# Performance work log

Hardware: AMD Instinct MI355X
Metric: run time of the kernel (lower is better)

## Reference

```python
import jax, jax.numpy as jnp
import numpy as np

B, F, L, E = 65536, 64, 32, 512  # batch, n_feat, n_latent, n_embed
LN_EPS = 1e-5


def setup_inputs() -> dict:
    key = jax.random.key(0)
    ks = jax.random.split(key, 9)
    s1 = 1.0 / np.sqrt(L)
    return {
        "batch_factors": jax.random.uniform(ks[0], (B, F), dtype=jnp.float32),
        "w_raw": jax.random.normal(ks[1], (F,), dtype=jnp.float32),
        "W1": jax.random.normal(ks[2], (F, L, L), dtype=jnp.float32) * s1,
        "b1": jax.random.normal(ks[3], (F, L), dtype=jnp.float32) * 0.01,
        "gamma": jnp.ones((F, L), dtype=jnp.float32),
        "beta": jnp.zeros((F, L), dtype=jnp.float32),
        "W2": jax.random.normal(ks[4], (F, L, E), dtype=jnp.float32) * s1,
        "b2": jax.random.normal(ks[5], (F, E), dtype=jnp.float32) * 0.01,
    }


def reference(batch_factors, w_raw, W1, b1, gamma, beta, W2, b2):
    half = L // 2
    freqs = 0.1 * (2.0 ** jnp.arange(half, dtype=batch_factors.dtype))  # [L/2]
    x = batch_factors[..., None]                                        # [B,F,1]
    enc = jnp.concatenate([jnp.sin(freqs * x), jnp.cos(freqs * x)], axis=-1)  # [B,F,L]

    # per-feature Linear -> LayerNorm -> GELU (dropout is identity in eval)
    h = jnp.einsum('bfi,fij->bfj', enc, W1) + b1                        # [B,F,L]
    mu = jnp.mean(h, axis=-1, keepdims=True)
    var = jnp.var(h, axis=-1, keepdims=True)
    h = (h - mu) * jax.lax.rsqrt(var + LN_EPS) * gamma + beta
    h = jax.nn.gelu(h, approximate=False)

    # softmax-weighted sum of per-feature Linear(L->E) outputs, fused so the
    # [B,F,E] intermediate is never materialized:
    w = jax.nn.softmax(w_raw)                                           # [F]
    batch_embed = jnp.einsum('bfj,fje->be', h * w[None, :, None], W2) + w @ b2  # [B,E]
    return (batch_embed, w)
```

## Files before the change

### kernel.cpp

```cpp
#include <hip/hip_runtime.h>
#include <hip/hip_bf16.h>
#include <cstdint>

#define B_N 65536
#define F_N 64
#define L_N 32
#define E_N 512

typedef short bf16x8 __attribute__((ext_vector_type(8)));
typedef float f32x4 __attribute__((ext_vector_type(4)));

__device__ __forceinline__ float gelu_fast(float v) {
  float z = fabsf(v) * 0.7071067811865476f;
  float p = fmaf(z, fmaf(z, fmaf(z, fmaf(z, 0.078108f, 0.000972f),
                                 0.230389f), 0.278393f), 1.0f);
  float p2 = p * p;
  float p4 = p2 * p2;
  float er = 1.0f - __builtin_amdgcn_rcpf(p4);
  float half_er = copysignf(0.5f * er, v);
  return v * (0.5f + half_er);
}

__device__ __forceinline__ float gelu_exact(float v) {
  float z  = v * 0.7071067811865476f;
  float az = fabsf(z);
  float t  = __builtin_amdgcn_rcpf(fmaf(0.3275911f, az, 1.0f));
  float p  = t * fmaf(t, fmaf(t, fmaf(t, fmaf(t, 1.061405429f, -1.453152027f),
                                      1.421413741f), -0.284496736f), 0.254829592f);
  float e    = __expf(-z * z);
  float erfa = fmaf(-p, e, 1.0f);
  float er   = (z < 0.0f) ? -erfa : erfa;
  return v * fmaf(0.5f, er, 0.5f);
}

__global__ __launch_bounds__(256) void k_pre(const float* __restrict__ w_raw,
                                             const float* __restrict__ b2,
                                             const float* __restrict__ W1,
                                             const float* __restrict__ W2,
                                             float* __restrict__ wb2,
                                             float* __restrict__ out_tail,
                                             uint4* __restrict__ W1T,
                                             uint4* __restrict__ W2T) {
  __shared__ float ls[64 * 65];
  int bb = blockIdx.x, tid = threadIdx.x;
  float m = -1e30f;
  for (int i = 0; i < F_N; i++) m = fmaxf(m, w_raw[i]);
  float s = 0.f;
  for (int i = 0; i < F_N; i++) s += expf(w_raw[i] - m);
  float inv_s = 1.0f / s;

  if (bb < 2) {
    int e = bb * 256 + tid;
    float a = 0.f;
    for (int f = 0; f < F_N; f++)
      a = fmaf(expf(w_raw[f] - m) * inv_s, b2[f * E_N + e], a);
    wb2[e] = a;
    if (bb == 0 && tid < F_N) out_tail[tid] = expf(w_raw[tid] - m) * inv_s;
  } else if (bb < 18) {
    int f = (bb - 2) * 4 + (tid >> 6);
    int lane = tid & 63, quad = lane >> 4, r16 = lane & 15;
#pragma unroll
    for (int jt = 0; jt < 2; jt++) {
      union { __hip_bfloat162 p[4]; uint4 u; } pk;
#pragma unroll
      for (int d = 0; d < 4; d++) {
        float lo = W1[f * 1024 + (quad * 4 + d) * 32 + jt * 16 + r16];
        float hi = W1[f * 1024 + (16 + quad * 4 + d) * 32 + jt * 16 + r16];
        pk.p[d] = __float22bfloat162_rn(make_float2(lo, hi));
      }
      W1T[(f * 2 + jt) * 64 + lane] = pk.u;
    }
  } else {
    int blk = bb - 18;
    int kt = blk >> 3, et = blk & 7;
    int k0 = kt * 64, e0 = et * 64;
#pragma unroll
    for (int i = 0; i < 16; i++) {
      int idx = i * 256 + tid;
      int r = idx >> 6, c = idx & 63;
      float wrow = expf(w_raw[(k0 + r) >> 5] - m) * inv_s;
      ls[r * 65 + c] = W2[(size_t)(k0 + r) * E_N + e0 + c] * wrow;
    }
    __syncthreads();
#pragma unroll
    for (int i = 0; i < 2; i++) {
      int t = i * 256 + tid;
      int ko = t >> 6, e = t & 63;
      union { __hip_bfloat162 p[4]; uint4 u; } pk;
#pragma unroll
      for (int d = 0; d < 4; d++)
        pk.p[d] = __float22bfloat162_rn(make_float2(ls[(ko * 8 + 2 * d) * 65 + e],
                                                    ls[(ko * 8 + 2 * d + 1) * 65 + e]));
      W2T[(size_t)(kt * 8 + ko) * E_N + e0 + e] = pk.u;
    }
  }
}

__device__ __forceinline__ void enc_chunk(int c, int wave, int lane, int quad,
                                          int r16, const float* xs, uint4* hwb,
                                          const uint4* __restrict__ W1T,
                                          const float* __restrict__ b1,
                                          const float* __restrict__ gamma,
                                          const float* __restrict__ beta,
                                          float c_t) {
  int f = c * 8 + wave;
  bf16x8 a0 = __builtin_bit_cast(bf16x8, W1T[(f * 2 + 0) * 64 + lane]);
  bf16x8 a1 = __builtin_bit_cast(bf16x8, W1T[(f * 2 + 1) * 64 + lane]);
  f32x4 c0, c1;
  float gv[8], bev[8];
#pragma unroll
  for (int rr = 0; rr < 4; rr++) {
    c0[rr] = b1[f * 32 + quad * 4 + rr];
    c1[rr] = b1[f * 32 + 16 + quad * 4 + rr];
  }
#pragma unroll
  for (int q = 0; q < 8; q++) {
    int idx = f * 32 + (q >> 2) * 16 + quad * 4 + (q & 3);
    gv[q] = gamma[idx];
    bev[q] = beta[idx];
  }
  int swz = f & 31;
#pragma unroll
  for (int bt = 0; bt < 4; bt++) {
    float x = xs[f * 64 + ((bt * 16 + r16) ^ swz)];
    float y = x * c_t;
    y = y - floorf(y);
    float sv = __builtin_amdgcn_sinf(y);
    float cv = __builtin_amdgcn_cosf(y);
    float v[8];
    v[0] = sv; v[1] = cv;
#pragma unroll
    for (int d = 1; d < 4; d++) {
      float c2 = cv + cv;
      float sn = c2 * sv;
      float cn = fmaf(c2, cv, -1.0f);
      v[2 * d] = sn; v[2 * d + 1] = cn;
      sv = sn; cv = cn;
    }
    union { __hip_bfloat162 p[4]; bf16x8 r; } pk;
#pragma unroll
    for (int d = 0; d < 4; d++)
      pk.p[d] = __float22bfloat162_rn(make_float2(v[2 * d], v[2 * d + 1]));
    f32x4 e0 = __builtin_amdgcn_mfma_f32_16x16x32_bf16(a0, pk.r, c0, 0, 0, 0);
    f32x4 e1 = __builtin_amdgcn_mfma_f32_16x16x32_bf16(a1, pk.r, c1, 0, 0, 0);
    float h[8];
#pragma unroll
    for (int rr = 0; rr < 4; rr++) { h[rr] = e0[rr]; h[4 + rr] = e1[rr]; }
    float sum = 0.f;
#pragma unroll
    for (int q = 0; q < 8; q++) sum += h[q];
    sum += __shfl_xor(sum, 16);
    sum += __shfl_xor(sum, 32);
    float mu = sum * (1.0f / 32.0f);
    float var = 0.f;
#pragma unroll
    for (int q = 0; q < 8; q++) { h[q] -= mu; var = fmaf(h[q], h[q], var); }
    var += __shfl_xor(var, 16);
    var += __shfl_xor(var, 32);
    float rs = __builtin_amdgcn_rsqf(fmaf(var, (1.0f / 32.0f), 1e-5f));
#pragma unroll
    for (int q = 0; q < 8; q++) {
      float hn = fmaf(h[q] * rs, gv[q], bev[q]);
      h[q] = gelu_fast(hn);
    }
    int b_local = bt * 16 + r16;
#pragma unroll
    for (int jt = 0; jt < 2; jt++) {
      union { __hip_bfloat162 p[2]; uint2 u; } pw;
      pw.p[0] = __float22bfloat162_rn(make_float2(h[jt * 4 + 0], h[jt * 4 + 1]));
      pw.p[1] = __float22bfloat162_rn(make_float2(h[jt * 4 + 2], h[jt * 4 + 3]));
      int ko_local = wave * 4 + jt * 2 + (quad >> 1);
      *(uint2*)((char*)hwb + ((size_t)(ko_local * 64 + b_local) * 16 +
                              (quad & 1) * 8)) = pw.u;
    }
  }
}

__device__ __forceinline__ void gemm_chunk(int c, int n_base, int quad, int r16,
                                           const uint4* hwb,
                                           const uint4* __restrict__ W2T,
                                           f32x4 (&acc)[4][4]) {
#pragma unroll
  for (int s = 0; s < 8; s++) {
    bf16x8 af[4], bfr[4];
#pragma unroll
    for (int nt = 0; nt < 4; nt++)
      bfr[nt] = __builtin_bit_cast(
          bf16x8, W2T[(size_t)(c * 32 + s * 4 + quad) * E_N + n_base + nt * 16 + r16]);
#pragma unroll
    for (int mt = 0; mt < 4; mt++)
      af[mt] = __builtin_bit_cast(bf16x8, hwb[(s * 4 + quad) * 64 + mt * 16 + r16]);
#pragma unroll
    for (int mt = 0; mt < 4; mt++)
#pragma unroll
      for (int nt = 0; nt < 4; nt++)
        acc[mt][nt] = __builtin_amdgcn_mfma_f32_16x16x32_bf16(af[mt], bfr[nt],
                                                              acc[mt][nt], 0, 0, 0);
  }
}

__global__ __launch_bounds__(512, 4) void k_fused(const float* __restrict__ bf,
                                                  const uint4* __restrict__ W1T,
                                                  const float* __restrict__ b1,
                                                  const float* __restrict__ gamma,
                                                  const float* __restrict__ beta,
                                                  const uint4* __restrict__ W2T,
                                                  const float* __restrict__ wb2,
                                                  float* __restrict__ out) {
  __shared__ float xs[64 * 64];
  __shared__ uint4 hwA[32 * 64];
  __shared__ uint4 hwB[32 * 64];
  int tid = threadIdx.x;
  int b0 = blockIdx.x * 64;
#pragma unroll
  for (int i = 0; i < 8; i++) {
    int idx = i * 512 + tid;
    int f = idx & 63, b = idx >> 6;
    xs[f * 64 + (b ^ (f & 31))] =
        __builtin_nontemporal_load(bf + (size_t)b0 * F_N + idx);
  }
  int wave = tid >> 6, lane = tid & 63;
  int quad = lane >> 4, r16 = lane & 15;
  float c_t = 0.015915494309189535f;
  if (quad & 1) c_t *= 16.0f;
  if (quad & 2) c_t *= 256.0f;
  int n_base = wave * 64;

  f32x4 acc[4][4];
  f32x4 zero = {0.f, 0.f, 0.f, 0.f};
#pragma unroll
  for (int i = 0; i < 4; i++)
#pragma unroll
    for (int j = 0; j < 4; j++) acc[i][j] = zero;

  __syncthreads();
  enc_chunk(0, wave, lane, quad, r16, xs, hwA, W1T, b1, gamma, beta, c_t);
  __syncthreads();

  for (int cc = 0; cc < 4; ++cc) {
    gemm_chunk(cc * 2, n_base, quad, r16, hwA, W2T, acc);
    enc_chunk(cc * 2 + 1, wave, lane, quad, r16, xs, hwB, W1T, b1, gamma, beta,
              c_t);
    __syncthreads();
    gemm_chunk(cc * 2 + 1, n_base, quad, r16, hwB, W2T, acc);
    if (cc < 3)
      enc_chunk(cc * 2 + 2, wave, lane, quad, r16, xs, hwA, W1T, b1, gamma, beta,
                c_t);
    __syncthreads();
  }

  float biasv[4];
#pragma unroll
  for (int nt = 0; nt < 4; nt++) biasv[nt] = wb2[n_base + nt * 16 + r16];
#pragma unroll
  for (int mt = 0; mt < 4; mt++) {
#pragma unroll
    for (int rr = 0; rr < 4; rr++) {
      size_t m = (size_t)b0 + mt * 16 + quad * 4 + rr;
      float* orow = out + m * E_N + n_base + r16;
#pragma unroll
      for (int nt = 0; nt < 4; nt++)
        __builtin_nontemporal_store(acc[mt][nt][rr] + biasv[nt], &orow[nt * 16]);
    }
  }
}

__global__ __launch_bounds__(64) void k_naive(const float* __restrict__ bf,
                                              const float* __restrict__ w_raw,
                                              const float* __restrict__ W1,
                                              const float* __restrict__ b1,
                                              const float* __restrict__ gamma,
                                              const float* __restrict__ beta,
                                              const float* __restrict__ W2,
                                              const float* __restrict__ b2,
                                              float* __restrict__ out) {
  int b = blockIdx.x;
  int lane = threadIdx.x;
  float m = -1e30f;
  for (int i = 0; i < F_N; i++) m = fmaxf(m, w_raw[i]);
  float s = 0.f;
  for (int i = 0; i < F_N; i++) s += expf(w_raw[i] - m);
  float inv_s = 1.0f / s;
  float acc[8];
#pragma unroll
  for (int r = 0; r < 8; r++) acc[r] = 0.f;
  __shared__ float hs[32];
  for (int f = 0; f < F_N; f++) {
    float wf = expf(w_raw[f] - m) * inv_s;
    __syncthreads();
    if (lane < 32) {
      float x = bf[(size_t)b * F_N + f];
      float t = x * 0.015915494309189535f;
      float h = b1[f * 32 + lane];
#pragma unroll
      for (int i = 0; i < 16; i++) {
        float y = t - floorf(t);
        h = fmaf(__builtin_amdgcn_sinf(y), W1[f * 1024 + i * 32 + lane], h);
        h = fmaf(__builtin_amdgcn_cosf(y), W1[f * 1024 + 512 + i * 32 + lane], h);
        t = t + t;
      }
      float sum = h;
#pragma unroll
      for (int msk = 1; msk < 32; msk <<= 1) sum += __shfl_xor(sum, msk, 64);
      float mu = sum * (1.0f / 32.0f);
      float d = h - mu;
      float sq = d * d;
#pragma unroll
      for (int msk = 1; msk < 32; msk <<= 1) sq += __shfl_xor(sq, msk, 64);
      float rs = __builtin_amdgcn_rsqf(fmaf(sq, (1.0f / 32.0f), 1e-5f));
      float hn = fmaf(d * rs, gamma[f * 32 + lane], beta[f * 32 + lane]);
      hs[lane] = gelu_exact(hn) * wf;
    }
    __syncthreads();
#pragma unroll
    for (int r = 0; r < 8; r++) {
      int e = r * 64 + lane;
      float a = fmaf(wf, b2[f * E_N + e], acc[r]);
      for (int j = 0; j < 32; j++)
        a = fmaf(hs[j], W2[(size_t)(f * 32 + j) * E_N + e], a);
      acc[r] = a;
    }
  }
#pragma unroll
  for (int r = 0; r < 8; r++) out[(size_t)b * E_N + r * 64 + lane] = acc[r];
  if (b == 0) out[(size_t)B_N * E_N + lane] = expf(w_raw[lane] - m) * inv_s;
}

extern "C" void kernel_launch(void* const* d_in, const int* in_sizes, int n_in,
                              void* d_out, int out_size, void* d_ws, size_t ws_size,
                              hipStream_t stream) {
  const float* bf    = (const float*)d_in[0];
  const float* w_raw = (const float*)d_in[1];
  const float* W1    = (const float*)d_in[2];
  const float* b1    = (const float*)d_in[3];
  const float* gamma = (const float*)d_in[4];
  const float* beta  = (const float*)d_in[5];
  const float* W2    = (const float*)d_in[6];
  const float* b2    = (const float*)d_in[7];
  float* out = (float*)d_out;

  const size_t W2T_BYTES = (size_t)256 * E_N * 16;
  const size_t W_OFF     = W2T_BYTES;
  const size_t WB2_OFF   = W_OFF + 256;
  const size_t W1T_OFF   = WB2_OFF + 4096;
  const size_t NEED      = W1T_OFF + 131072;

  if (ws_size < NEED) {
    k_naive<<<B_N, 64, 0, stream>>>(bf, w_raw, W1, b1, gamma, beta, W2, b2, out);
    return;
  }
  char* ws = (char*)d_ws;
  uint4* W2T = (uint4*)ws;
  float* wb2 = (float*)(ws + WB2_OFF);
  uint4* W1T = (uint4*)(ws + W1T_OFF);

  k_pre<<<274, 256, 0, stream>>>(w_raw, b2, W1, W2, wb2,
                                 out + (size_t)B_N * E_N, W1T, W2T);
  k_fused<<<B_N / 64, 512, 0, stream>>>(bf, W1T, b1, gamma, beta, W2T, wb2, out);
}
```

Before: 335.4 us.

## Interleave encoder slices into W2 GEMM loop for MFMA/VALU overlap

Splits the encoder stage into a parameter-load part and a per-batch-tile part, then runs one encoder batch tile after every second GEMM k-step inside the same loop. The goal is to overlap the VALU-heavy sin/cos, LayerNorm and GELU work with the MFMA-bound W2 GEMM within each wave, so both units stay busy. The final chunk runs the GEMM alone, which drops the last __syncthreads. The cost is higher register pressure from keeping encoder state live alongside the 16 accumulators, which could cause spills or lower occupancy.

```diff
diff --git a/kernel.cpp b/kernel.cpp
--- a/kernel.cpp
+++ b/kernel.cpp
@@ -96,106 +96,124 @@
   }
 }
 
-__device__ __forceinline__ void enc_chunk(int c, int wave, int lane, int quad,
-                                          int r16, const float* xs, uint4* hwb,
-                                          const uint4* __restrict__ W1T,
-                                          const float* __restrict__ b1,
-                                          const float* __restrict__ gamma,
-                                          const float* __restrict__ beta,
-                                          float c_t) {
-  int f = c * 8 + wave;
-  bf16x8 a0 = __builtin_bit_cast(bf16x8, W1T[(f * 2 + 0) * 64 + lane]);
-  bf16x8 a1 = __builtin_bit_cast(bf16x8, W1T[(f * 2 + 1) * 64 + lane]);
+struct EncSt {
+  bf16x8 a0, a1;
   f32x4 c0, c1;
   float gv[8], bev[8];
+  int f, swz;
+};
+
+__device__ __forceinline__ void enc_load(EncSt& st, int c, int wave, int quad,
+                                         int r16, int lane,
+                                         const uint4* __restrict__ W1T,
+                                         const float* __restrict__ b1,
+                                         const float* __restrict__ gamma,
+                                         const float* __restrict__ beta) {
+  int f = c * 8 + wave;
+  st.f = f;
+  st.swz = f & 31;
+  st.a0 = __builtin_bit_cast(bf16x8, W1T[(f * 2 + 0) * 64 + lane]);
+  st.a1 = __builtin_bit_cast(bf16x8, W1T[(f * 2 + 1) * 64 + lane]);
 #pragma unroll
   for (int rr = 0; rr < 4; rr++) {
-    c0[rr] = b1[f * 32 + quad * 4 + rr];
-    c1[rr] = b1[f * 32 + 16 + quad * 4 + rr];
+    st.c0[rr] = b1[f * 32 + quad * 4 + rr];
+    st.c1[rr] = b1[f * 32 + 16 + quad * 4 + rr];
   }
 #pragma unroll
   for (int q = 0; q < 8; q++) {
     int idx = f * 32 + (q >> 2) * 16 + quad * 4 + (q & 3);
-    gv[q] = gamma[idx];
-    bev[q] = beta[idx];
-  }
-  int swz = f & 31;
-#pragma unroll
-  for (int bt = 0; bt < 4; bt++) {
-    float x = xs[f * 64 + ((bt * 16 + r16) ^ swz)];
-    float y = x * c_t;
-    y = y - floorf(y);
-    float sv = __builtin_amdgcn_sinf(y);
-    float cv = __builtin_amdgcn_cosf(y);
-    float v[8];
-    v[0] = sv; v[1] = cv;
-#pragma unroll
-    for (int d = 1; d < 4; d++) {
-      float c2 = cv + cv;
-      float sn = c2 * sv;
-      float cn = fmaf(c2, cv, -1.0f);
-      v[2 * d] = sn; v[2 * d + 1] = cn;
-      sv = sn; cv = cn;
-    }
-    union { __hip_bfloat162 p[4]; bf16x8 r; } pk;
-#pragma unroll
-    for (int d = 0; d < 4; d++)
-      pk.p[d] = __float22bfloat162_rn(make_float2(v[2 * d], v[2 * d + 1]));
-    f32x4 e0 = __builtin_amdgcn_mfma_f32_16x16x32_bf16(a0, pk.r, c0, 0, 0, 0);
-    f32x4 e1 = __builtin_amdgcn_mfma_f32_16x16x32_bf16(a1, pk.r, c1, 0, 0, 0);
-    float h[8];
-#pragma unroll
-    for (int rr = 0; rr < 4; rr++) { h[rr] = e0[rr]; h[4 + rr] = e1[rr]; }
-    float sum = 0.f;
-#pragma unroll
-    for (int q = 0; q < 8; q++) sum += h[q];
-    sum += __shfl_xor(sum, 16);
-    sum += __shfl_xor(sum, 32);
-    float mu = sum * (1.0f / 32.0f);
-    float var = 0.f;
-#pragma unroll
-    for (int q = 0; q < 8; q++) { h[q] -= mu; var = fmaf(h[q], h[q], var); }
-    var += __shfl_xor(var, 16);
-    var += __shfl_xor(var, 32);
-    float rs = __builtin_amdgcn_rsqf(fmaf(var, (1.0f / 32.0f), 1e-5f));
-#pragma unroll
-    for (int q = 0; q < 8; q++) {
-      float hn = fmaf(h[q] * rs, gv[q], bev[q]);
-      h[q] = gelu_fast(hn);
-    }
-    int b_local = bt * 16 + r16;
-#pragma unroll
-    for (int jt = 0; jt < 2; jt++) {
-      union { __hip_bfloat162 p[2]; uint2 u; } pw;
-      pw.p[0] = __float22bfloat162_rn(make_float2(h[jt * 4 + 0], h[jt * 4 + 1]));
-      pw.p[1] = __float22bfloat162_rn(make_float2(h[jt * 4 + 2], h[jt * 4 + 3]));
-      int ko_local = wave * 4 + jt * 2 + (quad >> 1);
-      *(uint2*)((char*)hwb + ((size_t)(ko_local * 64 + b_local) * 16 +
-                              (quad & 1) * 8)) = pw.u;
-    }
-  }
-}
-
-__device__ __forceinline__ void gemm_chunk(int c, int n_base, int quad, int r16,
-                                           const uint4* hwb,
-                                           const uint4* __restrict__ W2T,
-                                           f32x4 (&acc)[4][4]) {
+    st.gv[q] = gamma[idx];
+    st.bev[q] = beta[idx];
+  }
+}
+
+__device__ __forceinline__ void enc_bt(const EncSt& st, int bt, int wave,
+                                       int quad, int r16, const float* xs,
+                                       uint4* hwb, float c_t) {
+  float x = xs[st.f * 64 + ((bt * 16 + r16) ^ st.swz)];
+  float y = x * c_t;
+  y = y - floorf(y);
+  float sv = __builtin_amdgcn_sinf(y);
+  float cv = __builtin_amdgcn_cosf(y);
+  float v[8];
+  v[0] = sv; v[1] = cv;
+#pragma unroll
+  for (int d = 1; d < 4; d++) {
+    float c2 = cv + cv;
+    float sn = c2 * sv;
+    float cn = fmaf(c2, cv, -1.0f);
+    v[2 * d] = sn; v[2 * d + 1] = cn;
+    sv = sn; cv = cn;
+  }
+  union { __hip_bfloat162 p[4]; bf16x8 r; } pk;
+#pragma unroll
+  for (int d = 0; d < 4; d++)
+    pk.p[d] = __float22bfloat162_rn(make_float2(v[2 * d], v[2 * d + 1]));
+  f32x4 e0 = __builtin_amdgcn_mfma_f32_16x16x32_bf16(st.a0, pk.r, st.c0, 0, 0, 0);
+  f32x4 e1 = __builtin_amdgcn_mfma_f32_16x16x32_bf16(st.a1, pk.r, st.c1, 0, 0, 0);
+  float h[8];
+#pragma unroll
+  for (int rr = 0; rr < 4; rr++) { h[rr] = e0[rr]; h[4 + rr] = e1[rr]; }
+  float sum = 0.f;
+#pragma unroll
+  for (int q = 0; q < 8; q++) sum += h[q];
+  sum += __shfl_xor(sum, 16);
+  sum += __shfl_xor(sum, 32);
+  float mu = sum * (1.0f / 32.0f);
+  float var = 0.f;
+#pragma unroll
+  for (int q = 0; q < 8; q++) { h[q] -= mu; var = fmaf(h[q], h[q], var); }
+  var += __shfl_xor(var, 16);
+  var += __shfl_xor(var, 32);
+  float rs = __builtin_amdgcn_rsqf(fmaf(var, (1.0f / 32.0f), 1e-5f));
+#pragma unroll
+  for (int q = 0; q < 8; q++) {
+    float hn = fmaf(h[q] * rs, st.gv[q], st.bev[q]);
+    h[q] = gelu_fast(hn);
+  }
+  int b_local = bt * 16 + r16;
+#pragma unroll
+  for (int jt = 0; jt < 2; jt++) {
+    union { __hip_bfloat162 p[2]; uint2 u; } pw;
+    pw.p[0] = __float22bfloat162_rn(make_float2(h[jt * 4 + 0], h[jt * 4 + 1]));
+    pw.p[1] = __float22bfloat162_rn(make_float2(h[jt * 4 + 2], h[jt * 4 + 3]));
+    int ko_local = wave * 4 + jt * 2 + (quad >> 1);
+    *(uint2*)((char*)hwb + ((size_t)(ko_local * 64 + b_local) * 16 +
+                            (quad & 1) * 8)) = pw.u;
+  }
+}
+
+template <bool ENC>
+__device__ __forceinline__ void fused_chunk(int cg, int ce, int wave, int lane,
+                                            int quad, int r16, int n_base,
+                                            const uint4* hw_rd, uint4* hw_wr,
+                                            const float* xs,
+                                            const uint4* __restrict__ W1T,
+                                            const uint4* __restrict__ W2T,
+                                            const float* __restrict__ b1,
+                                            const float* __restrict__ gamma,
+                                            const float* __restrict__ beta,
+                                            float c_t, f32x4 (&acc)[4][4]) {
+  EncSt st;
+  if (ENC) enc_load(st, ce, wave, quad, r16, lane, W1T, b1, gamma, beta);
 #pragma unroll
   for (int s = 0; s < 8; s++) {
     bf16x8 af[4], bfr[4];
 #pragma unroll
     for (int nt = 0; nt < 4; nt++)
       bfr[nt] = __builtin_bit_cast(
-          bf16x8, W2T[(size_t)(c * 32 + s * 4 + quad) * E_N + n_base + nt * 16 + r16]);
+          bf16x8,
+          W2T[(size_t)(cg * 32 + s * 4 + quad) * E_N + n_base + nt * 16 + r16]);
 #pragma unroll
     for (int mt = 0; mt < 4; mt++)
-      af[mt] = __builtin_bit_cast(bf16x8, hwb[(s * 4 + quad) * 64 + mt * 16 + r16]);
+      af[mt] = __builtin_bit_cast(bf16x8, hw_rd[(s * 4 + quad) * 64 + mt * 16 + r16]);
 #pragma unroll
     for (int mt = 0; mt < 4; mt++)
 #pragma unroll
       for (int nt = 0; nt < 4; nt++)
         acc[mt][nt] = __builtin_amdgcn_mfma_f32_16x16x32_bf16(af[mt], bfr[nt],
                                                               acc[mt][nt], 0, 0, 0);
+    if (ENC && (s & 1)) enc_bt(st, s >> 1, wave, quad, r16, xs, hw_wr, c_t);
   }
 }
 
@@ -234,19 +252,27 @@
     for (int j = 0; j < 4; j++) acc[i][j] = zero;
 
   __syncthreads();
-  enc_chunk(0, wave, lane, quad, r16, xs, hwA, W1T, b1, gamma, beta, c_t);
+  {
+    EncSt st0;
+    enc_load(st0, 0, wave, quad, r16, lane, W1T, b1, gamma, beta);
+#pragma unroll
+    for (int bt = 0; bt < 4; bt++)
+      enc_bt(st0, bt, wave, quad, r16, xs, hwA, c_t);
+  }
   __syncthreads();
 
   for (int cc = 0; cc < 4; ++cc) {
-    gemm_chunk(cc * 2, n_base, quad, r16, hwA, W2T, acc);
-    enc_chunk(cc * 2 + 1, wave, lane, quad, r16, xs, hwB, W1T, b1, gamma, beta,
-              c_t);
+    fused_chunk<true>(cc * 2, cc * 2 + 1, wave, lane, quad, r16, n_base, hwA,
+                      hwB, xs, W1T, W2T, b1, gamma, beta, c_t, acc);
     __syncthreads();
-    gemm_chunk(cc * 2 + 1, n_base, quad, r16, hwB, W2T, acc);
-    if (cc < 3)
-      enc_chunk(cc * 2 + 2, wave, lane, quad, r16, xs, hwA, W1T, b1, gamma, beta,
-                c_t);
-    __syncthreads();
+    if (cc < 3) {
+      fused_chunk<true>(cc * 2 + 1, cc * 2 + 2, wave, lane, quad, r16, n_base,
+                        hwB, hwA, xs, W1T, W2T, b1, gamma, beta, c_t, acc);
+      __syncthreads();
+    } else {
+      fused_chunk<false>(7, -1, wave, lane, quad, r16, n_base, hwB, hwA, xs,
+                         W1T, W2T, b1, gamma, beta, c_t, acc);
+    }
   }
 
   float biasv[4];
```

New measurement: 528.5 us. 57.6% more time.
